# Kernel optimization log

Measured on AMD Instinct MI355X. Metric: run time of the kernel, lower is better.

## Reference

```python
import jax, jax.numpy as jnp
import numpy as np

HEAD_DIM = 128
N_HEADS = 32
N_KV_HEADS = 8
ROPE_BASE = 500000.0
QK_EPS = 1e-6


def _rope_cos_sin(position_ids, head_dim, base, dtype):
    # position_ids: [B, S] int -> cos/sin [B, 1, S, head_dim]
    inv_freq = 1.0 / (base ** (jnp.arange(0, head_dim, 2, dtype=jnp.float32) / head_dim))
    freqs = position_ids.astype(jnp.float32)[..., None] * inv_freq  # [B, S, D/2]
    emb = jnp.concatenate([freqs, freqs], axis=-1)  # [B, S, D]
    return jnp.cos(emb).astype(dtype)[:, None], jnp.sin(emb).astype(dtype)[:, None]


def _rotate_half(x):
    x1, x2 = jnp.split(x, 2, axis=-1)
    return jnp.concatenate([-x2, x1], axis=-1)


def _qk_norm(x, scale, eps):
    # L2 norm (not RMS): scale * x / (||x||_2 + eps)
    norm = jnp.sqrt(jnp.sum(x * x, axis=-1, keepdims=True))
    return scale * x / (norm + eps)


def setup_inputs() -> dict:
    key = jax.random.key(0)
    ks = jax.random.split(key, 7)
    B, S, H = 1, 2048, 4096
    kv_dim = N_KV_HEADS * HEAD_DIM
    return {
        "hidden_states": jax.random.normal(ks[0], (B, S, H), dtype=jnp.float32),
        "position_ids": jnp.broadcast_to(jnp.arange(S, dtype=jnp.int64 if jax.config.jax_enable_x64 else jnp.int32), (B, S)),
        "Wq": jax.random.normal(ks[1], (H, H), dtype=jnp.float32) * (H ** -0.5),
        "Wk": jax.random.normal(ks[2], (kv_dim, H), dtype=jnp.float32) * (H ** -0.5),
        "Wv": jax.random.normal(ks[3], (kv_dim, H), dtype=jnp.float32) * (H ** -0.5),
        "Wo": jax.random.normal(ks[4], (H, H), dtype=jnp.float32) * (H ** -0.5),
        "q_scale": jnp.ones((HEAD_DIM,), dtype=jnp.float32),
        "k_scale": jnp.ones((HEAD_DIM,), dtype=jnp.float32),
    }


def reference(hidden_states, position_ids, Wq, Wk, Wv, Wo, q_scale, k_scale):
    B, S, H = hidden_states.shape
    scaling = 1.0 / np.sqrt(HEAD_DIM)

    # projections (torch Linear: y = x @ W.T)
    q = (hidden_states @ Wq.T).reshape(B, S, N_HEADS, HEAD_DIM).transpose(0, 2, 1, 3)
    k = (hidden_states @ Wk.T).reshape(B, S, N_KV_HEADS, HEAD_DIM).transpose(0, 2, 1, 3)
    v = (hidden_states @ Wv.T).reshape(B, S, N_KV_HEADS, HEAD_DIM).transpose(0, 2, 1, 3)

    cos, sin = _rope_cos_sin(position_ids, HEAD_DIM, ROPE_BASE, q.dtype)
    q = q * cos + _rotate_half(q) * sin
    k = k * cos + _rotate_half(k) * sin

    q = _qk_norm(q, q_scale, QK_EPS)
    k = _qk_norm(k, k_scale, QK_EPS)

    # GQA: repeat kv heads to match query heads
    n_rep = N_HEADS // N_KV_HEADS
    k = jnp.repeat(k, n_rep, axis=1)  # [B, n_heads, S, D]
    v = jnp.repeat(v, n_rep, axis=1)

    # causal SDPA
    scores = jnp.einsum("bhqd,bhkd->bhqk", q, k) * scaling
    causal = jnp.tril(jnp.ones((S, S), dtype=bool))
    scores = jnp.where(causal, scores, jnp.finfo(scores.dtype).min)
    attn = jax.nn.softmax(scores, axis=-1)
    out = jnp.einsum("bhqk,bhkd->bhqd", attn, v)  # [B, H, S, D]

    out = out.transpose(0, 2, 1, 3).reshape(B, S, H)
    return out @ Wo.T
```

## Files before the change

kernel.cpp:

```cpp
#include <hip/hip_runtime.h>
#include <math.h>

typedef unsigned short u16;
typedef unsigned int u32;
typedef __attribute__((ext_vector_type(8))) short bf16x8;
typedef __attribute__((ext_vector_type(4))) float f32x4;

#define S_LEN 2048
#define HID 4096
#define NH 32
#define NKV 8
#define HD 128
#define QS 6144

__device__ __forceinline__ u16 f2bf(float f) {
  u32 u = __float_as_uint(f);
  u32 r = (u + 0x7FFFu + ((u >> 16) & 1u)) >> 16;
  return (u16)r;
}
__device__ __forceinline__ float bf2f(u16 v) {
  return __uint_as_float(((u32)v) << 16);
}
__device__ __forceinline__ f32x4 mfma16(bf16x8 a, bf16x8 b, f32x4 c) {
  return __builtin_amdgcn_mfma_f32_16x16x32_bf16(a, b, c, 0, 0, 0);
}
__device__ __forceinline__ void async16(const u16* g, u16* l) {
  __builtin_amdgcn_global_load_lds(
      (__attribute__((address_space(1))) void*)g,
      (__attribute__((address_space(3))) void*)l, 16, 0, 0);
}
#if __has_builtin(__builtin_amdgcn_exp2f)
#define EXP2(x) __builtin_amdgcn_exp2f(x)
#else
#define EXP2(x) exp2f(x)
#endif

__global__ __launch_bounds__(256) void conv_all(
    const float* __restrict__ hs, const float* __restrict__ wq,
    const float* __restrict__ wk, const float* __restrict__ wv,
    const float* __restrict__ wo, u16* __restrict__ dhs, u16* __restrict__ dwq,
    u16* __restrict__ dwk, u16* __restrict__ dwv, u16* __restrict__ dwo) {
  int i = blockIdx.x * 256 + threadIdx.x;
  const float* src;
  u16* dst;
  int off;
  if (i < 2097152) { src = hs; dst = dhs; off = 0; }
  else if (i < 6291456) { src = wq; dst = dwq; off = 2097152; }
  else if (i < 7340032) { src = wk; dst = dwk; off = 6291456; }
  else if (i < 8388608) { src = wv; dst = dwv; off = 7340032; }
  else { src = wo; dst = dwo; off = 8388608; }
  int j = i - off;
  float4 v = ((const float4*)src)[j];
  ushort4 o;
  o.x = f2bf(v.x); o.y = f2bf(v.y); o.z = f2bf(v.z); o.w = f2bf(v.w);
  ((ushort4*)dst)[j] = o;
}


#define VMC(n) asm volatile("s_waitcnt vmcnt(" #n ")" ::: "memory")

#define LDA(qi, d)                                                         \
  {                                                                        \
    const u16* p_ = As + (d)*16384 + (wm * 64 + (qi)*32 + cl) * 64;        \
    _Pragma("unroll") for (int ii = 0; ii < 2; ii++)                       \
        _Pragma("unroll") for (int kk = 0; kk < 2; kk++)                   \
            a0[ii][kk] =                                                   \
        *(const bf16x8*)(p_ + ii * 1024 + ((c0 ^ (kk << 2)) << 3));        \
  }

#define LDB(dst, qj, d)                                                    \
  {                                                                        \
    const u16* p_ =                                                        \
        Bs + (d)*BSTR + (wn * (BN / 2) + (qj) * (BN / 4) + cl) * 64;       \
    _Pragma("unroll") for (int jj = 0; jj < NJ; jj++)                      \
        _Pragma("unroll") for (int kk = 0; kk < 2; kk++)                   \
            dst[jj][kk] =                                                  \
        *(const bf16x8*)(p_ + jj * 1024 + ((c0 ^ (kk << 2)) << 3));        \
  }

#define MM(qi, qj, bsrc)                                                   \
  {                                                                        \
    _Pragma("unroll") for (int ii = 0; ii < 2; ii++)                       \
        _Pragma("unroll") for (int jj = 0; jj < NJ; jj++)                  \
            _Pragma("unroll") for (int kk = 0; kk < 2; kk++)               \
                acc[(qi)*2 + ii][(qj)*NJ + jj] = mfma16(                   \
                    a0[ii][kk], bsrc[jj][kk], acc[(qi)*2 + ii][(qj)*NJ + jj]); \
  }

#define PH(MMA)                                                  \
  {                                                              \
    __builtin_amdgcn_s_barrier();                                \
    asm volatile("s_waitcnt lgkmcnt(0)" ::: "memory");           \
    __builtin_amdgcn_sched_barrier(0);                           \
    __builtin_amdgcn_s_setprio(1);                               \
    MMA;                                                         \
    __builtin_amdgcn_s_setprio(0);                               \
    __builtin_amdgcn_sched_barrier(0);                           \
    __builtin_amdgcn_s_barrier();                                \
  }

#define VMCNJ()                       \
  {                                   \
    if constexpr (NJ == 2) VMC(2);    \
    else VMC(3);                      \
  }

template <int NJ>
__global__ __launch_bounds__(512, 2) void gemm8p(
    const u16* __restrict__ A, const u16* __restrict__ B,
    u16* __restrict__ Cb, float* __restrict__ Cf, int N, int K) {
  constexpr int BN = NJ * 64;
  constexpr int BSTR = BN * 64;
  extern __shared__ u16 lds[];
  u16* As = lds;
  u16* Bs = lds + 32768;
  const int tid = threadIdx.x;
  const int lane = tid & 63, wv = tid >> 6;
  const int cl = lane & 15, qd = lane >> 4;
  const int wm = wv >> 1, wn = wv & 1;
  const int c0 = qd ^ (cl & 7);

  const int cpx = gridDim.x >> 3;
  const int swz = (blockIdx.x & 7) * cpx + (blockIdx.x >> 3);
  const int m0 = (swz & 7) * 256;
  const int n0 = (swz >> 3) * BN;

  u32 aof[4], bof[NJ];
#pragma unroll
  for (int q = 0; q < 4; q++) {
    int r = q * 64 + wv * 8 + (lane >> 3);
    int c = (lane & 7) ^ (r & 7);
    aof[q] = (u32)(m0 + r) * K + c * 8;
  }
#pragma unroll
  for (int q = 0; q < NJ; q++) {
    int r = q * 64 + wv * 8 + (lane >> 3);
    int c = (lane & 7) ^ (r & 7);
    bof[q] = (u32)(n0 + r) * K + c * 8;
  }
  const int sbo = wv * 512;

  auto STA = [&](int t, int d, int ra) {
    async16(A + (size_t)t * 64 + aof[ra], As + d * 16384 + ra * 4096 + sbo);
  };
  auto STB = [&](int t, int d, int rb) {
    async16(B + (size_t)t * 64 + bof[rb], Bs + d * BSTR + rb * 4096 + sbo);
  };

  f32x4 acc[4][2 * NJ];
  f32x4 zz = {0.f, 0.f, 0.f, 0.f};
#pragma unroll
  for (int i = 0; i < 4; i++)
#pragma unroll
    for (int j = 0; j < 2 * NJ; j++) acc[i][j] = zz;
  bf16x8 a0[2][2], b0[NJ][2], b1[NJ][2];

  const int NT = K >> 6;

  STA(0, 0, 0); STA(0, 0, 1); STA(0, 0, 2); STA(0, 0, 3);
  STB(0, 0, 0); STB(0, 0, 1);
  if constexpr (NJ == 3) STB(0, 0, 2);
  STB(1, 1, 0); STB(1, 1, 1);
  if constexpr (NJ == 3) STB(1, 1, 2);
  VMCNJ();
  __builtin_amdgcn_sched_barrier(0);
  __builtin_amdgcn_s_barrier();

  for (int it = 0; it < (NT >> 1); ++it) {
    const int t = it * 2;
    const bool s2 = (t + 2) < NT;
    LDA(0, 0); LDB(b0, 0, 0);
    STA(t + 1, 1, 0); STA(t + 1, 1, 1);
    PH(MM(0, 0, b0));
    LDB(b1, 1, 0);
    STA(t + 1, 1, 2); STA(t + 1, 1, 3);
    PH(MM(0, 1, b1));
    LDA(1, 0);
    if (s2) { STB(t + 2, 0, 0); STB(t + 2, 0, 1); }
    PH(MM(1, 0, b0));
    if (s2) {
      if constexpr (NJ == 3) STB(t + 2, 0, 2);
      VMCNJ();
    } else {
      VMC(0);
    }
    PH(MM(1, 1, b1));
    LDA(0, 1); LDB(b0, 0, 1);
    if (s2) { STA(t + 2, 0, 0); STA(t + 2, 0, 1); }
    PH(MM(0, 0, b0));
    LDB(b1, 1, 1);
    if (s2) { STA(t + 2, 0, 2); STA(t + 2, 0, 3); }
    PH(MM(0, 1, b1));
    LDA(1, 1);
    if (s2) { STB(t + 3, 1, 0); STB(t + 3, 1, 1); }
    PH(MM(1, 0, b0));
    if (s2) {
      if constexpr (NJ == 3) STB(t + 3, 1, 2);
      VMCNJ();
    } else {
      VMC(0);
    }
    PH(MM(1, 1, b1));
  }

#pragma unroll
  for (int i = 0; i < 4; i++)
#pragma unroll
    for (int j = 0; j < 2 * NJ; j++) {
      int row = m0 + wm * 64 + i * 16 + qd * 4;
      int col = n0 + wn * (BN / 2) + (j / NJ) * (BN / 4) + (j % NJ) * 16 + cl;
#pragma unroll
      for (int r = 0; r < 4; r++) {
        float v = acc[i][j][r];
        if (Cb) Cb[(size_t)(row + r) * N + col] = f2bf(v);
        else    Cf[(size_t)(row + r) * N + col] = v;
      }
    }
}

__global__ __launch_bounds__(256) void rope_l2norm(
    u16* __restrict__ x, const int* __restrict__ pos_ids,
    const float* __restrict__ scale, int hmask, int hshift, int stride) {
  const int lane = threadIdx.x & 63;
  const int wv = threadIdx.x >> 6;
  const int idx = blockIdx.x * 4 + wv;
  const int s = idx >> hshift;
  const int h = idx & hmask;
  u16* p = x + (size_t)s * stride + h * HD;
  const float pos = (float)pos_ids[s];
  const float inv = expf((float)lane * -0.20503692777194264f);
  float sn, cs;
  sincosf(pos * inv, &sn, &cs);
  float a = bf2f(p[lane]);
  float b = bf2f(p[lane + 64]);
  float ra = a * cs - b * sn;
  float rb = b * cs + a * sn;
  float ss = ra * ra + rb * rb;
#pragma unroll
  for (int off = 32; off >= 1; off >>= 1) ss += __shfl_xor(ss, off, 64);
  float rd = 1.0f / (sqrtf(ss) + 1e-6f);
  p[lane] = f2bf(scale[lane] * ra * rd);
  p[lane + 64] = f2bf(scale[lane + 64] * rb * rd);
}

__global__ __launch_bounds__(256) void transpose_v(const u16* __restrict__ v,
                                                   u16* __restrict__ vt) {
  __shared__ u16 t[64][65];
  const int r = threadIdx.x >> 6;
  const int c = threadIdx.x & 63;
  const int s0 = blockIdx.x * 64, d0 = blockIdx.y * 64;
#pragma unroll
  for (int i = 0; i < 16; i++) {
    int row = i * 4 + r;
    t[row][c] = v[(size_t)(s0 + row) * QS + d0 + c];
  }
  __syncthreads();
#pragma unroll
  for (int i = 0; i < 16; i++) {
    int row = i * 4 + r;
    vt[(size_t)(d0 + row) * S_LEN + s0 + c] = t[c][row];
  }
}

#define PLD 68

__global__ __launch_bounds__(512) void flash_attn(
    const u16* __restrict__ QKV, const u16* __restrict__ Vt,
    u16* __restrict__ O) {
  __shared__ u16 Ks[64 * 128];
  __shared__ u16 Vs[128 * 64];
  __shared__ u16 Ps[128 * PLD];
  const int tid = threadIdx.x;
  const int lane = tid & 63, wv = tid >> 6;
  const int cl = lane & 15, qd = lane >> 4;
  const int h = blockIdx.y;
  const int kvh = h >> 2;
  const float es = 0.12751629240081506f;

  const u16* Kbase = QKV + 4096 + kvh * HD;
  const u16* Vbase = Vt + (size_t)kvh * HD * S_LEN;

  for (int half = 0; half < 2; half++) {
    const int qbi = half ? (15 - blockIdx.x) : blockIdx.x;
    const int q0 = qbi * 128;

    bf16x8 aQ[4];
    {
      const u16* qrow =
          QKV + (size_t)(q0 + wv * 16 + cl) * QS + h * HD + qd * 8;
#pragma unroll
      for (int kk = 0; kk < 4; kk++) aQ[kk] = *(const bf16x8*)(qrow + kk * 32);
    }

    f32x4 oacc[8];
    f32x4 zz = {0.f, 0.f, 0.f, 0.f};
#pragma unroll
    for (int n = 0; n < 8; n++) oacc[n] = zz;
    float lsum[4] = {0.f, 0.f, 0.f, 0.f};

    const int row_min = q0 + wv * 16;
    const int ktmax = 2 * qbi + 1;

    for (int kt = 0; kt <= ktmax; kt++) {
      __syncthreads();
#pragma unroll
      for (int q = 0; q < 2; q++) {
        int c = q * 512 + wv * 64 + lane;
        int kr = c >> 4, kg = (c & 15) ^ (kr & 15);
        async16(Kbase + (size_t)(kt * 64 + kr) * QS + kg * 8,
                Ks + (q * 512 + wv * 64) * 8);
        int vr = c >> 3, vg = (c & 7) ^ (vr & 7);
        async16(Vbase + (size_t)vr * S_LEN + kt * 64 + vg * 8,
                Vs + (q * 512 + wv * 64) * 8);
      }
      __syncthreads();

      if (kt * 64 <= row_min + 15) {
        f32x4 sacc[4];
#pragma unroll
        for (int j = 0; j < 4; j++) sacc[j] = zz;
#pragma unroll
        for (int j = 0; j < 4; j++) {
          int row = j * 16 + cl;
#pragma unroll
          for (int kk = 0; kk < 4; kk++) {
            int ch = (kk * 4 + qd) ^ (row & 15);
            bf16x8 bK = *(const bf16x8*)&Ks[row * 128 + ch * 8];
            sacc[j] = mfma16(aQ[kk], bK, sacc[j]);
          }
        }

        float pm[4][4];
        if (kt * 64 + 63 > row_min) {
          const int grow = row_min + qd * 4;
#pragma unroll
          for (int j = 0; j < 4; j++) {
            int gcol = kt * 64 + j * 16 + cl;
#pragma unroll
            for (int r = 0; r < 4; r++)
              pm[j][r] = (gcol <= grow + r) ? EXP2(sacc[j][r] * es) : 0.f;
          }
        } else {
#pragma unroll
          for (int j = 0; j < 4; j++)
#pragma unroll
            for (int r = 0; r < 4; r++) pm[j][r] = EXP2(sacc[j][r] * es);
        }
#pragma unroll
        for (int j = 0; j < 4; j++)
#pragma unroll
          for (int r = 0; r < 4; r++) lsum[r] += pm[j][r];

#pragma unroll
        for (int j = 0; j < 4; j++)
#pragma unroll
          for (int r = 0; r < 4; r++)
            Ps[(wv * 16 + qd * 4 + r) * PLD + j * 16 + cl] = f2bf(pm[j][r]);
        __asm__ volatile("s_waitcnt lgkmcnt(0)" ::: "memory");

#pragma unroll
        for (int kk = 0; kk < 2; kk++) {
          bf16x8 aP =
              *(const bf16x8*)&Ps[(wv * 16 + cl) * PLD + kk * 32 + qd * 8];
#pragma unroll
          for (int n = 0; n < 8; n++) {
            int row = n * 16 + cl;
            int ch = (kk * 4 + qd) ^ (row & 7);
            bf16x8 bV = *(const bf16x8*)&Vs[row * 64 + ch * 8];
            oacc[n] = mfma16(aP, bV, oacc[n]);
          }
        }
      }
    }

#pragma unroll
    for (int r = 0; r < 4; r++) {
#pragma unroll
      for (int off = 8; off >= 1; off >>= 1)
        lsum[r] += __shfl_xor(lsum[r], off, 64);
    }
#pragma unroll
    for (int r = 0; r < 4; r++) {
      float il = 1.0f / lsum[r];
      int row = row_min + qd * 4 + r;
#pragma unroll
      for (int n = 0; n < 8; n++)
        O[(size_t)row * HID + h * HD + n * 16 + cl] = f2bf(oacc[n][r] * il);
    }
  }
}

extern "C" void kernel_launch(void* const* d_in, const int* in_sizes, int n_in,
                              void* d_out, int out_size, void* d_ws, size_t ws_size,
                              hipStream_t stream) {
  const float* hs = (const float*)d_in[0];
  const int* pos = (const int*)d_in[1];
  const float* Wq = (const float*)d_in[2];
  const float* Wk = (const float*)d_in[3];
  const float* Wv = (const float*)d_in[4];
  const float* Wo = (const float*)d_in[5];
  const float* qsc = (const float*)d_in[6];
  const float* ksc = (const float*)d_in[7];
  float* out = (float*)d_out;
  char* ws = (char*)d_ws;
  const size_t MB = 1u << 20;

  u16* hs_b  = (u16*)(ws + 0 * MB);
  u16* wq_b  = (u16*)(ws + 16 * MB);
  u16* wk_b  = (u16*)(ws + 48 * MB);
  u16* wv_b  = (u16*)(ws + 56 * MB);
  u16* qkv_b = (u16*)(ws + 64 * MB);
  u16* vt_b  = (u16*)(ws + 88 * MB);
  u16* wo_b  = (u16*)(ws + 92 * MB);
  u16* o_b   = hs_b;

  static bool attr_set = false;
  if (!attr_set) {
    hipFuncSetAttribute(reinterpret_cast<const void*>(&gemm8p<3>),
                        hipFuncAttributeMaxDynamicSharedMemorySize, 114688);
    hipFuncSetAttribute(reinterpret_cast<const void*>(&gemm8p<2>),
                        hipFuncAttributeMaxDynamicSharedMemorySize, 98304);
    attr_set = true;
  }

  conv_all<<<49152, 256, 0, stream>>>(hs, Wq, Wk, Wv, Wo,
                                      hs_b, wq_b, wk_b, wv_b, wo_b);

  gemm8p<3><<<dim3(8 * (QS / 192)), 512, 114688, stream>>>(
      hs_b, wq_b, qkv_b, nullptr, QS, HID);

  rope_l2norm<<<S_LEN * NH / 4, 256, 0, stream>>>(qkv_b, pos, qsc, NH - 1, 5, QS);
  rope_l2norm<<<S_LEN * NKV / 4, 256, 0, stream>>>(qkv_b + 4096, pos, ksc, NKV - 1, 3, QS);
  transpose_v<<<dim3(S_LEN / 64, (NKV * HD) / 64), 256, 0, stream>>>(qkv_b + 5120, vt_b);

  flash_attn<<<dim3(8, NH), 512, 0, stream>>>(qkv_b, vt_b, o_b);

  gemm8p<2><<<dim3(8 * (HID / 128)), 512, 98304, stream>>>(
      o_b, wo_b, nullptr, out, HID, HID);
}
```

Baseline: 454.9 us.

## Double-buffer LDS fragments in GEMM and K/V tiles in flash attention

The GEMM main loop now keeps separate A and B register fragment sets and issues the LDS reads for the next phase before the current MFMA block. Partial lgkmcnt waits let those reads overlap the matrix math. Flash attention moves to dynamic shared memory with two K/V buffers, so the async load of the next key tile overlaps compute on the current one, replacing two syncthreads per tile with a single wait and barrier. This costs more registers and more LDS per block, which can lower occupancy. The hand-tuned wait counts must also match the exact number of outstanding operations.

```diff
diff --git a/kernel.cpp b/kernel.cpp
--- a/kernel.cpp
+++ b/kernel.cpp
@@ -34,6 +34,13 @@
 #else
 #define EXP2(x) exp2f(x)
 #endif
+
+#define VMC(n) asm volatile("s_waitcnt vmcnt(" #n ")" ::: "memory")
+#define LGKM(n) asm volatile("s_waitcnt lgkmcnt(" #n ")" ::: "memory")
+#define SB __builtin_amdgcn_sched_barrier(0)
+#define BAR __builtin_amdgcn_s_barrier()
+#define P1 __builtin_amdgcn_s_setprio(1)
+#define P0 __builtin_amdgcn_s_setprio(0)
 
 __global__ __launch_bounds__(256) void conv_all(
     const float* __restrict__ hs, const float* __restrict__ wq,
@@ -57,18 +64,16 @@
 }
 
 
-#define VMC(n) asm volatile("s_waitcnt vmcnt(" #n ")" ::: "memory")
-
-#define LDA(qi, d)                                                         \
+#define DSA(dst, qi, d)                                                    \
   {                                                                        \
     const u16* p_ = As + (d)*16384 + (wm * 64 + (qi)*32 + cl) * 64;        \
     _Pragma("unroll") for (int ii = 0; ii < 2; ii++)                       \
         _Pragma("unroll") for (int kk = 0; kk < 2; kk++)                   \
-            a0[ii][kk] =                                                   \
+            dst[ii][kk] =                                                  \
         *(const bf16x8*)(p_ + ii * 1024 + ((c0 ^ (kk << 2)) << 3));        \
   }
 
-#define LDB(dst, qj, d)                                                    \
+#define DSB(dst, qj, d)                                                    \
   {                                                                        \
     const u16* p_ =                                                        \
         Bs + (d)*BSTR + (wn * (BN / 2) + (qj) * (BN / 4) + cl) * 64;       \
@@ -78,32 +83,30 @@
         *(const bf16x8*)(p_ + jj * 1024 + ((c0 ^ (kk << 2)) << 3));        \
   }
 
-#define MM(qi, qj, bsrc)                                                   \
+#define MM(qi, qj, asrc, bsrc)                                             \
   {                                                                        \
     _Pragma("unroll") for (int ii = 0; ii < 2; ii++)                       \
         _Pragma("unroll") for (int jj = 0; jj < NJ; jj++)                  \
             _Pragma("unroll") for (int kk = 0; kk < 2; kk++)               \
-                acc[(qi)*2 + ii][(qj)*NJ + jj] = mfma16(                   \
-                    a0[ii][kk], bsrc[jj][kk], acc[(qi)*2 + ii][(qj)*NJ + jj]); \
-  }
-
-#define PH(MMA)                                                  \
-  {                                                              \
-    __builtin_amdgcn_s_barrier();                                \
-    asm volatile("s_waitcnt lgkmcnt(0)" ::: "memory");           \
-    __builtin_amdgcn_sched_barrier(0);                           \
-    __builtin_amdgcn_s_setprio(1);                               \
-    MMA;                                                         \
-    __builtin_amdgcn_s_setprio(0);                               \
-    __builtin_amdgcn_sched_barrier(0);                           \
-    __builtin_amdgcn_s_barrier();                                \
-  }
-
-#define VMCNJ()                       \
-  {                                   \
-    if constexpr (NJ == 2) VMC(2);    \
-    else VMC(3);                      \
-  }
+                acc[(qi)*2 + ii][(qj)*NJ + jj] =                           \
+        mfma16(asrc[ii][kk], bsrc[jj][kk], acc[(qi)*2 + ii][(qj)*NJ + jj]);\
+  }
+
+#define LGKM_NB()                           \
+  do {                                      \
+    if constexpr (NJ == 3) LGKM(6);         \
+    else LGKM(4);                           \
+  } while (0)
+#define LGKM_NB4()                          \
+  do {                                      \
+    if constexpr (NJ == 3) LGKM(10);        \
+    else LGKM(8);                           \
+  } while (0)
+#define VMCNJ()                             \
+  do {                                      \
+    if constexpr (NJ == 3) VMC(3);          \
+    else VMC(2);                            \
+  } while (0)
 
 template <int NJ>
 __global__ __launch_bounds__(512, 2) void gemm8p(
@@ -140,11 +143,11 @@
   }
   const int sbo = wv * 512;
 
-  auto STA = [&](int t, int d, int ra) {
-    async16(A + (size_t)t * 64 + aof[ra], As + d * 16384 + ra * 4096 + sbo);
+  auto STA = [&](int tt, int d, int ra) {
+    async16(A + (size_t)tt * 64 + aof[ra], As + d * 16384 + ra * 4096 + sbo);
   };
-  auto STB = [&](int t, int d, int rb) {
-    async16(B + (size_t)t * 64 + bof[rb], Bs + d * BSTR + rb * 4096 + sbo);
+  auto STB = [&](int tt, int d, int rb) {
+    async16(B + (size_t)tt * 64 + bof[rb], Bs + d * BSTR + rb * 4096 + sbo);
   };
 
   f32x4 acc[4][2 * NJ];
@@ -153,7 +156,7 @@
   for (int i = 0; i < 4; i++)
 #pragma unroll
     for (int j = 0; j < 2 * NJ; j++) acc[i][j] = zz;
-  bf16x8 a0[2][2], b0[NJ][2], b1[NJ][2];
+  bf16x8 A0r[2][2], A1r[2][2], B0r[NJ][2], B1r[NJ][2];
 
   const int NT = K >> 6;
 
@@ -163,44 +166,48 @@
   STB(1, 1, 0); STB(1, 1, 1);
   if constexpr (NJ == 3) STB(1, 1, 2);
   VMCNJ();
-  __builtin_amdgcn_sched_barrier(0);
-  __builtin_amdgcn_s_barrier();
+  SB;
+  BAR;
+  DSA(A0r, 0, 0); DSB(B0r, 0, 0);
+  SB; LGKM(0); SB;
 
   for (int it = 0; it < (NT >> 1); ++it) {
     const int t = it * 2;
     const bool s2 = (t + 2) < NT;
-    LDA(0, 0); LDB(b0, 0, 0);
     STA(t + 1, 1, 0); STA(t + 1, 1, 1);
-    PH(MM(0, 0, b0));
-    LDB(b1, 1, 0);
+    BAR; DSB(B1r, 1, 0); SB; LGKM_NB(); SB;
+    P1; MM(0, 0, A0r, B0r); P0; SB; BAR;
     STA(t + 1, 1, 2); STA(t + 1, 1, 3);
-    PH(MM(0, 1, b1));
-    LDA(1, 0);
+    BAR; DSA(A1r, 1, 0); SB; LGKM(4); SB;
+    P1; MM(0, 1, A0r, B1r); P0; SB; BAR;
     if (s2) { STB(t + 2, 0, 0); STB(t + 2, 0, 1); }
-    PH(MM(1, 0, b0));
+    BAR; SB; LGKM(0); SB;
+    P1; MM(1, 0, A1r, B0r); P0; SB; BAR;
     if (s2) {
       if constexpr (NJ == 3) STB(t + 2, 0, 2);
       VMCNJ();
     } else {
       VMC(0);
     }
-    PH(MM(1, 1, b1));
-    LDA(0, 1); LDB(b0, 0, 1);
+    BAR; DSB(B0r, 0, 1); DSA(A0r, 0, 1); SB; LGKM_NB4(); SB;
+    P1; MM(1, 1, A1r, B1r); P0; SB; BAR;
     if (s2) { STA(t + 2, 0, 0); STA(t + 2, 0, 1); }
-    PH(MM(0, 0, b0));
-    LDB(b1, 1, 1);
+    BAR; DSB(B1r, 1, 1); SB; LGKM_NB(); SB;
+    P1; MM(0, 0, A0r, B0r); P0; SB; BAR;
     if (s2) { STA(t + 2, 0, 2); STA(t + 2, 0, 3); }
-    PH(MM(0, 1, b1));
-    LDA(1, 1);
+    BAR; DSA(A1r, 1, 1); SB; LGKM(4); SB;
+    P1; MM(0, 1, A0r, B1r); P0; SB; BAR;
     if (s2) { STB(t + 3, 1, 0); STB(t + 3, 1, 1); }
-    PH(MM(1, 0, b0));
+    BAR; SB; LGKM(0); SB;
+    P1; MM(1, 0, A1r, B0r); P0; SB; BAR;
     if (s2) {
       if constexpr (NJ == 3) STB(t + 3, 1, 2);
       VMCNJ();
     } else {
       VMC(0);
     }
-    PH(MM(1, 1, b1));
+    BAR; DSB(B0r, 0, 0); DSA(A0r, 0, 0); SB; LGKM_NB4(); SB;
+    P1; MM(1, 1, A1r, B1r); P0; SB; BAR;
   }
 
 #pragma unroll
@@ -267,9 +274,10 @@
 __global__ __launch_bounds__(512) void flash_attn(
     const u16* __restrict__ QKV, const u16* __restrict__ Vt,
     u16* __restrict__ O) {
-  __shared__ u16 Ks[64 * 128];
-  __shared__ u16 Vs[128 * 64];
-  __shared__ u16 Ps[128 * PLD];
+  extern __shared__ u16 alds[];
+  u16* Ks = alds;
+  u16* Vs = alds + 16384;
+  u16* Ps = alds + 32768;
   const int tid = threadIdx.x;
   const int lane = tid & 63, wv = tid >> 6;
   const int cl = lane & 15, qd = lane >> 4;
@@ -280,8 +288,21 @@
   const u16* Kbase = QKV + 4096 + kvh * HD;
   const u16* Vbase = Vt + (size_t)kvh * HD * S_LEN;
 
+  auto stage = [&](int kt, int d) {
+#pragma unroll
+    for (int q = 0; q < 2; q++) {
+      int c = q * 512 + wv * 64 + lane;
+      int kr = c >> 4, kg = (c & 15) ^ (kr & 15);
+      async16(Kbase + (size_t)(kt * 64 + kr) * QS + kg * 8,
+              Ks + d * 8192 + (q * 512 + wv * 64) * 8);
+      int vr = c >> 3, vg = (c & 7) ^ (vr & 7);
+      async16(Vbase + (size_t)vr * S_LEN + kt * 64 + vg * 8,
+              Vs + d * 8192 + (q * 512 + wv * 64) * 8);
+    }
+  };
+
   for (int half = 0; half < 2; half++) {
-    const int qbi = half ? (15 - blockIdx.x) : blockIdx.x;
+    const int qbi = half ? (15 - (int)blockIdx.x) : (int)blockIdx.x;
     const int q0 = qbi * 128;
 
     bf16x8 aQ[4];
@@ -301,19 +322,16 @@
     const int row_min = q0 + wv * 16;
     const int ktmax = 2 * qbi + 1;
 
+    int cur = 0;
+    stage(0, 0);
     for (int kt = 0; kt <= ktmax; kt++) {
-      __syncthreads();
-#pragma unroll
-      for (int q = 0; q < 2; q++) {
-        int c = q * 512 + wv * 64 + lane;
-        int kr = c >> 4, kg = (c & 15) ^ (kr & 15);
-        async16(Kbase + (size_t)(kt * 64 + kr) * QS + kg * 8,
-                Ks + (q * 512 + wv * 64) * 8);
-        int vr = c >> 3, vg = (c & 7) ^ (vr & 7);
-        async16(Vbase + (size_t)vr * S_LEN + kt * 64 + vg * 8,
-                Vs + (q * 512 + wv * 64) * 8);
+      if (kt < ktmax) stage(kt + 1, cur ^ 1);
+      if (kt == 0) {
+        VMC(4);
+        SB;
+        BAR;
       }
-      __syncthreads();
+      const int koff = cur * 8192;
 
       if (kt * 64 <= row_min + 15) {
         f32x4 sacc[4];
@@ -325,7 +343,7 @@
 #pragma unroll
           for (int kk = 0; kk < 4; kk++) {
             int ch = (kk * 4 + qd) ^ (row & 15);
-            bf16x8 bK = *(const bf16x8*)&Ks[row * 128 + ch * 8];
+            bf16x8 bK = *(const bf16x8*)&Ks[koff + row * 128 + ch * 8];
             sacc[j] = mfma16(aQ[kk], bK, sacc[j]);
           }
         }
@@ -366,11 +384,16 @@
           for (int n = 0; n < 8; n++) {
             int row = n * 16 + cl;
             int ch = (kk * 4 + qd) ^ (row & 7);
-            bf16x8 bV = *(const bf16x8*)&Vs[row * 64 + ch * 8];
+            bf16x8 bV = *(const bf16x8*)&Vs[koff + row * 64 + ch * 8];
             oacc[n] = mfma16(aP, bV, oacc[n]);
           }
         }
       }
+
+      VMC(0);
+      SB;
+      BAR;
+      cur ^= 1;
     }
 
 #pragma unroll
@@ -420,6 +443,8 @@
                         hipFuncAttributeMaxDynamicSharedMemorySize, 114688);
     hipFuncSetAttribute(reinterpret_cast<const void*>(&gemm8p<2>),
                         hipFuncAttributeMaxDynamicSharedMemorySize, 98304);
+    hipFuncSetAttribute(reinterpret_cast<const void*>(&flash_attn),
+                        hipFuncAttributeMaxDynamicSharedMemorySize, 82944);
     attr_set = true;
   }
 
@@ -433,7 +458,7 @@
   rope_l2norm<<<S_LEN * NKV / 4, 256, 0, stream>>>(qkv_b + 4096, pos, ksc, NKV - 1, 3, QS);
   transpose_v<<<dim3(S_LEN / 64, (NKV * HD) / 64), 256, 0, stream>>>(qkv_b + 5120, vt_b);
 
-  flash_attn<<<dim3(8, NH), 512, 0, stream>>>(qkv_b, vt_b, o_b);
+  flash_attn<<<dim3(8, NH), 512, 82944, stream>>>(qkv_b, vt_b, o_b);
 
   gemm8p<2><<<dim3(8 * (HID / 128)), 512, 98304, stream>>>(
       o_b, wo_b, nullptr, out, HID, HID);
```

Measured after the change: 465.8 us. +2.4%, slower.
